# Optimization experiments

Hardware: AMD Instinct MI355X
Metric: run time of the kernel (lower is better)

Reference implementation:

```python
import jax, jax.numpy as jnp
import numpy as np
from jax import lax

DIM = 64
HEADS = 8
B, H, W = 4, 256, 256


def layer_norm(x, w, b):
    # WithBias LayerNorm over channel dim (dim=1 of NCHW), per-pixel
    mu = jnp.mean(x, axis=1, keepdims=True)
    var = jnp.mean((x - mu) ** 2, axis=1, keepdims=True)
    xn = (x - mu) / jnp.sqrt(var + 1e-5)
    return xn * w[None, :, None, None] + b[None, :, None, None]


def conv1x1(x, w, b=None):
    out = jnp.einsum('oc,bchw->bohw', w, x)
    if b is not None:
        out = out + b[None, :, None, None]
    return out


def dwconv3x3(x, w):
    # w: [C,1,3,3], depthwise (groups=C), stride 1, pad 1
    return lax.conv_general_dilated(
        x, w, window_strides=(1, 1), padding=((1, 1), (1, 1)),
        feature_group_count=x.shape[1],
        dimension_numbers=('NCHW', 'OIHW', 'NCHW'))


def modulation(v, y, mw, mb):
    # mw: [4, C, C] = [scale0, scale1, shift0, shift1]; mb: [4, C]
    s = conv1x1(jax.nn.leaky_relu(conv1x1(y, mw[0], mb[0]), 0.1), mw[1], mb[1])
    t = conv1x1(jax.nn.leaky_relu(conv1x1(y, mw[2], mb[2]), 0.1), mw[3], mb[3])
    return v * (s + 1.0) + t


def _heads(t):
    b, c, h, w = t.shape
    return t.reshape(b, HEADS, c // HEADS, h * w)


def channel_attn(q, k, v, temp):
    b, c, h, w = v.shape
    q, k, v = _heads(q), _heads(k), _heads(v)  # b, head, ch, hw
    q = q / jnp.maximum(jnp.linalg.norm(q, axis=-1, keepdims=True), 1e-12)
    k = k / jnp.maximum(jnp.linalg.norm(k, axis=-1, keepdims=True), 1e-12)
    attn = jnp.einsum('bhcn,bhdn->bhcd', q, k) * temp[None]  # small CxC
    attn = jax.nn.softmax(attn, axis=-1)
    out = jnp.einsum('bhcd,bhdn->bhcn', attn, v)
    return out.reshape(b, c, h, w)


def setup_inputs() -> dict:
    key = jax.random.key(0)
    ks = jax.random.split(key, 24)
    sc = 0.05
    d = {
        'x': jax.random.normal(ks[0], (B, DIM, H, W), jnp.float32),
        'y': jax.random.normal(ks[1], (B, DIM, H, W), jnp.float32),
        'ln_w': jnp.ones((DIM,), jnp.float32),
        'ln_b': jnp.zeros((DIM,), jnp.float32),
        'temp': jnp.ones((HEADS, 1, 1), jnp.float32),
        'kv1_w': jax.random.normal(ks[2], (2 * DIM, DIM), jnp.float32) * sc,
        'kvdw1_w': jax.random.normal(ks[3], (2 * DIM, 1, 3, 3), jnp.float32) * sc,
        'q1_w': jax.random.normal(ks[4], (DIM, DIM), jnp.float32) * sc,
        'qdw1_w': jax.random.normal(ks[5], (DIM, 1, 3, 3), jnp.float32) * sc,
        'po1_w': jax.random.normal(ks[6], (DIM, DIM), jnp.float32) * sc,
        'kv2_w': jax.random.normal(ks[7], (2 * DIM, DIM), jnp.float32) * sc,
        'kvdw2_w': jax.random.normal(ks[8], (2 * DIM, 1, 3, 3), jnp.float32) * sc,
        'q2_w': jax.random.normal(ks[9], (DIM, DIM), jnp.float32) * sc,
        'qdw2_w': jax.random.normal(ks[10], (DIM, 1, 3, 3), jnp.float32) * sc,
        'po2_w': jax.random.normal(ks[11], (DIM, DIM), jnp.float32) * sc,
        'mm1_w': jax.random.normal(ks[12], (4, DIM, DIM), jnp.float32) * sc,
        'mm1_b': jnp.zeros((4, DIM), jnp.float32),
        'mm2_w': jax.random.normal(ks[13], (4, DIM, DIM), jnp.float32) * sc,
        'mm2_b': jnp.zeros((4, DIM), jnp.float32),
    }
    return d


def reference(x, y, ln_w, ln_b, temp,
              kv1_w, kvdw1_w, q1_w, qdw1_w, po1_w,
              kv2_w, kvdw2_w, q2_w, qdw2_w, po2_w,
              mm1_w, mm1_b, mm2_w, mm2_b):
    x1 = layer_norm(x, ln_w, ln_b)
    y1 = layer_norm(y, ln_w, ln_b)  # original reuses self.norm1 for both

    # branch 1: kv from x1, q from y1, v modulated by x, residual y
    kv1 = dwconv3x3(conv1x1(x1, kv1_w), kvdw1_w)
    k1, v1 = jnp.split(kv1, 2, axis=1)
    q1 = dwconv3x3(conv1x1(y1, q1_w), qdw1_w)
    v1 = modulation(v1, x, mm1_w, mm1_b)
    out1 = conv1x1(channel_attn(q1, k1, v1, temp), po1_w) + y

    # branch 2: kv from y1, q from x1, v modulated by y, residual x
    kv2 = dwconv3x3(conv1x1(y1, kv2_w), kvdw2_w)
    k2, v2 = jnp.split(kv2, 2, axis=1)
    q2 = dwconv3x3(conv1x1(x1, q2_w), qdw2_w)
    v2 = modulation(v2, y, mm2_w, mm2_b)
    out2 = conv1x1(channel_attn(q2, k2, v2, temp), po2_w) + x

    return (out1, out2)
```

## Files before the change

kernel.cpp:

```cpp
#include <hip/hip_runtime.h>
#include <hip/hip_bf16.h>

#define HW 65536
#define BATCH 4
#define NPIX (BATCH*HW)

typedef unsigned short u16;
typedef unsigned int   u32;
typedef __attribute__((ext_vector_type(8))) short bh8;
typedef __attribute__((ext_vector_type(4))) float f4;

__device__ __forceinline__ float b2f(u16 u){
    u32 i = ((u32)u) << 16; float f; __builtin_memcpy(&f, &i, 4); return f;
}
__device__ __forceinline__ u16 f2b(float f){
    __hip_bfloat16 h = __float2bfloat16(f); u16 u; __builtin_memcpy(&u, &h, 2); return u;
}

__device__ __forceinline__ f4 mfma16(bh8 a, bh8 b, f4 c){
    return __builtin_amdgcn_mfma_f32_16x16x32_bf16(a, b, c, 0, 0, 0);
}

struct CvtJob { const float* src; u16* dst; int n; const float* cs; };
struct SetupArgs {
    CvtJob j[12];
    const float* kvw[2]; const float* qw[2];
    const float* lnw; const float* lnb;
    float* sums; float* lnc;
};
__global__ __launch_bounds__(256) void setup_kernel(SetupArgs S){
    int blk = blockIdx.x;
    if (blk < 12){
        const CvtJob J = S.j[blk];
        if (J.cs){
            for (int i = threadIdx.x; i < J.n; i += 256) J.dst[i] = f2b(J.src[i] * J.cs[i & 63]);
        } else {
            for (int i = threadIdx.x; i < J.n; i += 256) J.dst[i] = f2b(J.src[i]);
        }
        return;
    }
    int pb = blk - 12;
    if (pb == 0){
        for (int i = threadIdx.x; i < 5120; i += 256) S.sums[i] = 0.f;
    } else if (pb <= 2){
        const float* W = S.kvw[pb-1];
        float* rs = S.lnc + (pb-1)*256;
        int o = threadIdx.x;
        if (o < 128){
            float a = 0.f, bb = 0.f;
            for (int c = 0; c < 64; c++){
                float wv = W[o*64 + c];
                a = fmaf(wv, S.lnw[c], a); bb = fmaf(wv, S.lnb[c], bb);
            }
            rs[o] = a; rs[128 + o] = bb;
        }
    } else {
        const float* W = S.qw[pb-3];
        float* rs = S.lnc + 512 + (pb-3)*128;
        int o = threadIdx.x;
        if (o < 64){
            float a = 0.f, bb = 0.f;
            for (int c = 0; c < 64; c++){
                float wv = W[o*64 + c];
                a = fmaf(wv, S.lnw[c], a); bb = fmaf(wv, S.lnb[c], bb);
            }
            rs[o] = a; rs[64 + o] = bb;
        }
    }
}

struct GemmDual {
    const float* in[2];
    const u16* wa[2];
    const float* rs[2]; const float* rb[2];
    u16* outLo[2]; u16* outHi[2];
};
template<int MT>
__global__ __launch_bounds__(256) void gemmln_kernel(GemmDual G){
    constexpr int KD = 64;
    constexpr int NW = MT*16*KD;
    __shared__ u16 wl[NW];
    int seg = blockIdx.x >> 10, tile = blockIdx.x & 1023;
    int w = threadIdx.x >> 6, lane = threadIdx.x & 63;
    int quad = lane >> 4, l16 = lane & 15;
    int b = tile >> 8;
    int pbase = ((tile & 255) << 8) + (w << 6) + (l16 << 2);

    const float* in = G.in[seg];
    f4 fin[8];
    #pragma unroll
    for (int j = 0; j < 8; j++)
        fin[j] = *(const f4*)(in + ((size_t)b*64 + quad*8 + j)*HW + pbase);

    {
        const u16* W = G.wa[seg];
        for (int i = threadIdx.x; i < NW/8; i += 256){
            int row = i >> 3, ch = i & 7;
            uint4 v = *(const uint4*)(W + row*KD + ch*8);
            *(uint4*)(wl + row*KD + ((ch ^ (row & 7)) << 3)) = v;
        }
    }
    __syncthreads();

    f4 fin2[8];
    #pragma unroll
    for (int j = 0; j < 8; j++)
        fin2[j] = *(const f4*)(in + ((size_t)b*64 + 32 + quad*8 + j)*HW + pbase);

    float s1[4] = {0.f,0.f,0.f,0.f}, s2[4] = {0.f,0.f,0.f,0.f};
    f4 acc[MT][4];
    #pragma unroll
    for (int mi = 0; mi < MT; mi++)
        #pragma unroll
        for (int p = 0; p < 4; p++) acc[mi][p] = (f4){0.f,0.f,0.f,0.f};

    #pragma unroll
    for (int ks = 0; ks < 2; ks++){
        bh8 bfr[4];
        #pragma unroll
        for (int j = 0; j < 8; j++){
            f4 fv = (ks == 0) ? fin[j] : fin2[j];
            #pragma unroll
            for (int p = 0; p < 4; p++){
                float v = fv[p];
                s1[p] += v; s2[p] = fmaf(v, v, s2[p]);
                bfr[p][j] = (short)f2b(v);
            }
        }
        #pragma unroll
        for (int mi = 0; mi < MT; mi++){
            bh8 a;
            __builtin_memcpy(&a, wl + (mi*16 + l16)*KD + ((((ks<<2)+quad) ^ (l16 & 7)) << 3), 16);
            #pragma unroll
            for (int p = 0; p < 4; p++)
                acc[mi][p] = mfma16(a, bfr[p], acc[mi][p]);
        }
    }

    float mu[4], iv[4];
    #pragma unroll
    for (int p = 0; p < 4; p++){
        s1[p] += __shfl_xor(s1[p], 16); s1[p] += __shfl_xor(s1[p], 32);
        s2[p] += __shfl_xor(s2[p], 16); s2[p] += __shfl_xor(s2[p], 32);
        mu[p] = s1[p]*(1.f/64.f);
        iv[p] = rsqrtf(s2[p]*(1.f/64.f) - mu[p]*mu[p] + 1e-5f);
    }

    const float* rs = G.rs[seg]; const float* rb = G.rb[seg];
    u16* oLo = G.outLo[seg]; u16* oHi = G.outHi[seg];
    #pragma unroll
    for (int mi = 0; mi < MT; mi++)
    #pragma unroll
    for (int r = 0; r < 4; r++){
        int o = mi*16 + quad*4 + r;
        size_t pidx = ((size_t)b*64 + (o & 63))*HW + pbase;
        float rsv = rs[o], rbv = rb[o];
        float v0 = iv[0]*(acc[mi][0][r] - mu[0]*rsv) + rbv;
        float v1 = iv[1]*(acc[mi][1][r] - mu[1]*rsv) + rbv;
        float v2 = iv[2]*(acc[mi][2][r] - mu[2]*rsv) + rbv;
        float v3 = iv[3]*(acc[mi][3][r] - mu[3]*rsv) + rbv;
        uint2 st;
        st.x = (u32)f2b(v0) | ((u32)f2b(v1) << 16);
        st.y = (u32)f2b(v2) | ((u32)f2b(v3) << 16);
        u16* dst = (o < 64) ? oLo : oHi;
        *(uint2*)(dst + pidx) = st;
    }
}

struct Dw6 { const u16* in[6]; u16* out[6]; const float* w[6]; int choff[6]; };
__global__ __launch_bounds__(256) void dw6_kernel(Dw6 A){
    int seg = blockIdx.x >> 13;
    int lid = ((blockIdx.x & 8191) << 8) + threadIdx.x;
    const u16* inp = A.in[seg];
    u16* outp      = A.out[seg];
    const float* wd = A.w[seg];
    int choff      = A.choff[seg];
    int bc = lid >> 13;
    int n8 = lid & 8191;
    int h = n8 >> 5, c8 = (n8 & 31) << 3;
    const float* wc = wd + ((size_t)((bc & 63) + choff))*9;
    const u16* p = inp + (size_t)bc*HW;
    float row[3][10];
    #pragma unroll
    for (int r = 0; r < 3; r++){
        int hh = h - 1 + r;
        bool ok = (unsigned)hh < 256u;
        const u16* pr = p + hh*256 + c8;
        if (ok){
            uint4 m = *(const uint4*)pr;
            row[r][1] = b2f((u16)m.x); row[r][2] = b2f((u16)(m.x>>16));
            row[r][3] = b2f((u16)m.y); row[r][4] = b2f((u16)(m.y>>16));
            row[r][5] = b2f((u16)m.z); row[r][6] = b2f((u16)(m.z>>16));
            row[r][7] = b2f((u16)m.w); row[r][8] = b2f((u16)(m.w>>16));
            row[r][0] = (c8 > 0)   ? b2f(pr[-1]) : 0.f;
            row[r][9] = (c8 < 248) ? b2f(pr[8])  : 0.f;
        } else {
            #pragma unroll
            for (int j = 0; j < 10; j++) row[r][j] = 0.f;
        }
    }
    float o[8];
    #pragma unroll
    for (int i = 0; i < 8; i++){
        float a = 0.f;
        #pragma unroll
        for (int r = 0; r < 3; r++){
            a = fmaf(wc[r*3+0], row[r][i],   a);
            a = fmaf(wc[r*3+1], row[r][i+1], a);
            a = fmaf(wc[r*3+2], row[r][i+2], a);
        }
        o[i] = a;
    }
    uint4 st;
    st.x = (u32)f2b(o[0]) | ((u32)f2b(o[1])<<16);
    st.y = (u32)f2b(o[2]) | ((u32)f2b(o[3])<<16);
    st.z = (u32)f2b(o[4]) | ((u32)f2b(o[5])<<16);
    st.w = (u32)f2b(o[6]) | ((u32)f2b(o[7])<<16);
    *(uint4*)(outp + (size_t)bc*HW + h*256 + c8) = st;
}

#define NSL 64
struct AttnDual { const u16* q[2]; const u16* k[2]; float* sums; };
__global__ __launch_bounds__(256) void attn_part_kernel(AttnDual AD){
    int seg = blockIdx.x >> 11;
    int blk = blockIdx.x & 2047;
    int sl = blk & (NSL-1);
    int bh = blk >> 6;
    int b = bh >> 3, h = bh & 7;
    const u16* qp = AD.q[seg] + ((size_t)b*64 + h*8)*HW + sl*(HW/NSL);
    const u16* kp = AD.k[seg] + ((size_t)b*64 + h*8)*HW + sl*(HW/NSL);
    float acc[80];
    #pragma unroll
    for (int i = 0; i < 80; i++) acc[i] = 0.f;
    int n0 = threadIdx.x << 2;
    float qv[8][4], kw[8][4];
    #pragma unroll
    for (int i = 0; i < 8; i++){
        uint2 mq = *(const uint2*)(qp + (size_t)i*HW + n0);
        uint2 mk = *(const uint2*)(kp + (size_t)i*HW + n0);
        qv[i][0] = b2f((u16)(mq.x & 0xffffu)); qv[i][1] = b2f((u16)(mq.x >> 16));
        qv[i][2] = b2f((u16)(mq.y & 0xffffu)); qv[i][3] = b2f((u16)(mq.y >> 16));
        kw[i][0] = b2f((u16)(mk.x & 0xffffu)); kw[i][1] = b2f((u16)(mk.x >> 16));
        kw[i][2] = b2f((u16)(mk.y & 0xffffu)); kw[i][3] = b2f((u16)(mk.y >> 16));
    }
    #pragma unroll
    for (int i = 0; i < 8; i++){
        #pragma unroll
        for (int u = 0; u < 4; u++){
            acc[64+i] = fmaf(qv[i][u], qv[i][u], acc[64+i]);
            acc[72+i] = fmaf(kw[i][u], kw[i][u], acc[72+i]);
        }
        #pragma unroll
        for (int j = 0; j < 8; j++)
            #pragma unroll
            for (int u = 0; u < 4; u++)
                acc[i*8+j] = fmaf(qv[i][u], kw[j][u], acc[i*8+j]);
    }
    __shared__ float sred[4][80];
    int lane = threadIdx.x & 63, wv = threadIdx.x >> 6;
    #pragma unroll
    for (int t = 0; t < 80; t++){
        float r = acc[t];
        r += __shfl_down(r, 32); r += __shfl_down(r, 16); r += __shfl_down(r, 8);
        r += __shfl_down(r, 4);  r += __shfl_down(r, 2);  r += __shfl_down(r, 1);
        if (lane == 0) sred[wv][t] = r;
    }
    __syncthreads();
    if (threadIdx.x < 80){
        int t = threadIdx.x;
        atomicAdd(&AD.sums[seg*2560 + bh*80 + t], sred[0][t]+sred[1][t]+sred[2][t]+sred[3][t]);
    }
}

struct WeffDual { const float* sums; const float* temp; const float* po[2]; u16* weff[2]; };
__global__ __launch_bounds__(64) void weff_kernel(WeffDual WD){
    int seg = blockIdx.x >> 2;
    int b = blockIdx.x & 3;
    const float* po = WD.po[seg];
    u16* weff = WD.weff[seg];
    __shared__ float at[8][8][8];
    int t = threadIdx.x;
    {
        int h = t >> 3, i = t & 7;
        const float* f = WD.sums + seg*2560 + (b*8 + h)*80;
        float iq = 1.f / fmaxf(sqrtf(f[64+i]), 1e-12f);
        float tv = WD.temp[h];
        float row[8]; float m = -1e30f;
        #pragma unroll
        for (int j = 0; j < 8; j++){
            float ik = 1.f / fmaxf(sqrtf(f[72+j]), 1e-12f);
            row[j] = f[i*8+j]*iq*ik*tv;
            m = fmaxf(m, row[j]);
        }
        float s = 0.f;
        #pragma unroll
        for (int j = 0; j < 8; j++){ row[j] = expf(row[j]-m); s += row[j]; }
        float rsv = 1.f/s;
        #pragma unroll
        for (int j = 0; j < 8; j++) at[h][i][j] = row[j]*rsv;
    }
    __syncthreads();
    int o = t;
    for (int g = 0; g < 64; g++){
        int h = g >> 3, j = g & 7;
        float wv = 0.f;
        #pragma unroll
        for (int i = 0; i < 8; i++) wv = fmaf(po[o*64 + h*8 + i], at[h][i][j], wv);
        weff[b*4096 + o*64 + g] = f2b(wv);
    }
}

struct ModFinal {
    const float* in[2]; const u16* wa[2]; const u16* wb[2];
    const float* b0[2]; const float* b2[2]; const float* b1[2]; const float* b3[2];
    const u16* wf[2];
    const u16* v[2];
    const float* resid[2];
    float* out[2];
};
__global__ __launch_bounds__(256) void modfinal_kernel(ModFinal M){
    __shared__ u32 lds[128*128];
    int seg = blockIdx.x >> 10, tile = blockIdx.x & 1023;
    int w = threadIdx.x >> 6, lane = threadIdx.x & 63;
    int quad = lane >> 4, l16 = lane & 15;
    int b = tile >> 8;
    int pbase = ((tile & 255) << 8) + (w << 6) + (l16 << 2);
    int pp = ((w << 4) + l16) << 1;

    const float* in = M.in[seg];
    const u16* wa = M.wa[seg];

    f4 fin[8], fin2[8];
    #pragma unroll
    for (int j = 0; j < 8; j++)
        fin[j] = *(const f4*)(in + ((size_t)b*64 + quad*8 + j)*HW + pbase);
    #pragma unroll
    for (int j = 0; j < 8; j++)
        fin2[j] = *(const f4*)(in + ((size_t)b*64 + 32 + quad*8 + j)*HW + pbase);

    f4 acc[8][4];
    #pragma unroll
    for (int mi = 0; mi < 8; mi++)
        #pragma unroll
        for (int p = 0; p < 4; p++) acc[mi][p] = (f4){0.f,0.f,0.f,0.f};

    #pragma unroll
    for (int ks = 0; ks < 2; ks++){
        bh8 bfr[4];
        #pragma unroll
        for (int j = 0; j < 8; j++){
            f4 fv = (ks == 0) ? fin[j] : fin2[j];
            #pragma unroll
            for (int p = 0; p < 4; p++) bfr[p][j] = (short)f2b(fv[p]);
        }
        #pragma unroll
        for (int mi = 0; mi < 8; mi++){
            bh8 a;
            __builtin_memcpy(&a, wa + (mi*16 + l16)*64 + ks*32 + quad*8, 16);
            #pragma unroll
            for (int p = 0; p < 4; p++)
                acc[mi][p] = mfma16(a, bfr[p], acc[mi][p]);
        }
    }

    uint2 vpref[16];
    {
        const u16* vP = M.v[seg];
        #pragma unroll
        for (int mi = 0; mi < 4; mi++)
        #pragma unroll
        for (int r = 0; r < 4; r++)
            vpref[mi*4+r] = *(const uint2*)(vP + ((size_t)b*64 + mi*16 + quad*4 + r)*HW + pbase);
    }

    {
        const float* b0v = M.b0[seg]; const float* b2v = M.b2[seg];
        #pragma unroll
        for (int mi = 0; mi < 8; mi++)
        #pragma unroll
        for (int r = 0; r < 4; r++){
            int o = mi*16 + quad*4 + r;
            float bi = (o < 64) ? b0v[o] : b2v[o-64];
            float v0 = acc[mi][0][r] + bi; v0 = v0 > 0.f ? v0 : 0.1f*v0;
            float v1 = acc[mi][1][r] + bi; v1 = v1 > 0.f ? v1 : 0.1f*v1;
            float v2 = acc[mi][2][r] + bi; v2 = v2 > 0.f ? v2 : 0.1f*v2;
            float v3 = acc[mi][3][r] + bi; v3 = v3 > 0.f ? v3 : 0.1f*v3;
            uint2 st;
            st.x = (u32)f2b(v0) | ((u32)f2b(v1) << 16);
            st.y = (u32)f2b(v2) | ((u32)f2b(v3) << 16);
            *(uint2*)&lds[o*128 + ((pp + ((o>>2)&3)*8) & 127)] = st;
        }
    }
    __syncthreads();

    const u16* wb = M.wb[seg];
    f4 acc2[8][4];
    #pragma unroll
    for (int mi = 0; mi < 8; mi++)
        #pragma unroll
        for (int p = 0; p < 4; p++) acc2[mi][p] = (f4){0.f,0.f,0.f,0.f};
    #pragma unroll
    for (int ks = 0; ks < 4; ks++){
        int kb = ks*32 + quad*8;
        bh8 bfr[4];
        #pragma unroll
        for (int j = 0; j < 8; j++){
            int ch = kb + j;
            uint2 m = *(const uint2*)&lds[ch*128 + ((pp + ((ch>>2)&3)*8) & 127)];
            bfr[0][j] = (short)(m.x & 0xffffu);
            bfr[1][j] = (short)(m.x >> 16);
            bfr[2][j] = (short)(m.y & 0xffffu);
            bfr[3][j] = (short)(m.y >> 16);
        }
        #pragma unroll
        for (int mi = 0; mi < 8; mi++){
            if (mi < 4 ? (ks < 2) : (ks >= 2)){
                int ksl = (mi >= 4) ? ks - 2 : ks;
                bh8 a;
                __builtin_memcpy(&a, wb + (mi*16 + l16)*64 + ksl*32 + quad*8, 16);
                #pragma unroll
                for (int p = 0; p < 4; p++)
                    acc2[mi][p] = mfma16(a, bfr[p], acc2[mi][p]);
            }
        }
    }
    __syncthreads();

    {
        const float* b1v = M.b1[seg]; const float* b3v = M.b3[seg];
        #pragma unroll
        for (int mi = 0; mi < 4; mi++)
        #pragma unroll
        for (int r = 0; r < 4; r++){
            int o = mi*16 + quad*4 + r;
            uint2 vv = vpref[mi*4+r];
            float va[4] = { b2f((u16)(vv.x & 0xffffu)), b2f((u16)(vv.x >> 16)),
                            b2f((u16)(vv.y & 0xffffu)), b2f((u16)(vv.y >> 16)) };
            float ov[4];
            #pragma unroll
            for (int p = 0; p < 4; p++){
                float s = acc2[mi][p][r] + b1v[o];
                float t = acc2[mi+4][p][r] + b3v[o];
                ov[p] = va[p]*(s+1.f)+t;
            }
            uint2 st;
            st.x = (u32)f2b(ov[0]) | ((u32)f2b(ov[1]) << 16);
            st.y = (u32)f2b(ov[2]) | ((u32)f2b(ov[3]) << 16);
            *(uint2*)&lds[o*128 + ((pp + ((o>>2)&3)*8) & 127)] = st;
        }
    }
    f4 rpre[16];
    {
        const float* resid = M.resid[seg];
        #pragma unroll
        for (int mi = 0; mi < 4; mi++)
        #pragma unroll
        for (int r = 0; r < 4; r++)
            rpre[mi*4+r] = *(const f4*)(resid + ((size_t)b*64 + mi*16 + quad*4 + r)*HW + pbase);
    }
    __syncthreads();

    const u16* wf = M.wf[seg] + b*4096;
    f4 accF[4][4];
    #pragma unroll
    for (int mi = 0; mi < 4; mi++)
        #pragma unroll
        for (int p = 0; p < 4; p++) accF[mi][p] = (f4){0.f,0.f,0.f,0.f};
    #pragma unroll
    for (int ks = 0; ks < 2; ks++){
        int kb = ks*32 + quad*8;
        bh8 bfr[4];
        #pragma unroll
        for (int j = 0; j < 8; j++){
            int ch = kb + j;
            uint2 m = *(const uint2*)&lds[ch*128 + ((pp + ((ch>>2)&3)*8) & 127)];
            bfr[0][j] = (short)(m.x & 0xffffu);
            bfr[1][j] = (short)(m.x >> 16);
            bfr[2][j] = (short)(m.y & 0xffffu);
            bfr[3][j] = (short)(m.y >> 16);
        }
        #pragma unroll
        for (int mi = 0; mi < 4; mi++){
            bh8 a;
            __builtin_memcpy(&a, wf + (mi*16 + l16)*64 + ks*32 + quad*8, 16);
            #pragma unroll
            for (int p = 0; p < 4; p++)
                accF[mi][p] = mfma16(a, bfr[p], accF[mi][p]);
        }
    }
    {
        float* outF = M.out[seg];
        #pragma unroll
        for (int mi = 0; mi < 4; mi++)
        #pragma unroll
        for (int r = 0; r < 4; r++){
            int o = mi*16 + quad*4 + r;
            size_t pidx = ((size_t)b*64 + o)*HW + pbase;
            f4 rr = rpre[mi*4+r];
            f4 st;
            #pragma unroll
            for (int p = 0; p < 4; p++) st[p] = accF[mi][p][r] + rr[p];
            *(f4*)(outF + pidx) = st;
        }
    }
}

extern "C" void kernel_launch(void* const* d_in, const int* in_sizes, int n_in,
                              void* d_out, int out_size, void* d_ws, size_t ws_size,
                              hipStream_t stream){
    const float* x    = (const float*)d_in[0];
    const float* y    = (const float*)d_in[1];
    const float* ln_w = (const float*)d_in[2];
    const float* ln_b = (const float*)d_in[3];
    const float* temp = (const float*)d_in[4];
    const float* kv_w[2]   = {(const float*)d_in[5],  (const float*)d_in[10]};
    const float* kvdw_w[2] = {(const float*)d_in[6],  (const float*)d_in[11]};
    const float* q_w[2]    = {(const float*)d_in[7],  (const float*)d_in[12]};
    const float* qdw_w[2]  = {(const float*)d_in[8],  (const float*)d_in[13]};
    const float* po_w[2]   = {(const float*)d_in[9],  (const float*)d_in[14]};
    const float* mm_w[2]   = {(const float*)d_in[15], (const float*)d_in[17]};
    const float* mm_b[2]   = {(const float*)d_in[16], (const float*)d_in[18]};

    const size_t HPE = (size_t)BATCH*64*HW;
    u16* PL = (u16*)d_ws;
    u16* P[12];
    for (int i = 0; i < 12; i++) P[i] = PL + (size_t)i*HPE;
    float* sums = (float*)(PL + 12*HPE);
    float* lnc  = sums + 5120;
    u16* warena = (u16*)(lnc + 768);
    const int WKV[2] = {0, 8192}, WQ[2] = {16384, 20480};
    const int WMA[2] = {24576, 40960}, WMB[2] = {32768, 49152};
    const int WEFF[2] = {57344, 73728};

    size_t need = 12*HPE*2 + (5120+768)*4 + 90112*2;
    if (ws_size < need) return;

    SetupArgs S{};
    int nj = 0;
    auto add = [&](const float* s, u16* d, int n, const float* cs){ S.j[nj] = {s, d, n, cs}; nj++; };
    for (int br = 0; br < 2; br++){
        add(kv_w[br],        warena + WKV[br],        8192, ln_w);
        add(q_w[br],         warena + WQ[br],         4096, ln_w);
        add(mm_w[br],        warena + WMA[br],        4096, nullptr);
        add(mm_w[br]+8192,   warena + WMA[br] + 4096, 4096, nullptr);
        add(mm_w[br]+4096,   warena + WMB[br],        4096, nullptr);
        add(mm_w[br]+12288,  warena + WMB[br] + 4096, 4096, nullptr);
    }
    S.kvw[0] = kv_w[0]; S.kvw[1] = kv_w[1];
    S.qw[0]  = q_w[0];  S.qw[1]  = q_w[1];
    S.lnw = ln_w; S.lnb = ln_b; S.sums = sums; S.lnc = lnc;
    setup_kernel<<<17, 256, 0, stream>>>(S);

    const int GT = NPIX/256;

    GemmDual GK{};
    GK.in[0] = x; GK.in[1] = y;
    GK.wa[0] = warena + WKV[0]; GK.wa[1] = warena + WKV[1];
    GK.rs[0] = lnc;        GK.rb[0] = lnc + 128;
    GK.rs[1] = lnc + 256;  GK.rb[1] = lnc + 384;
    GK.outLo[0] = P[0]; GK.outHi[0] = P[1];
    GK.outLo[1] = P[2]; GK.outHi[1] = P[3];
    gemmln_kernel<8><<<2*GT, 256, 0, stream>>>(GK);

    GemmDual GQ{};
    GQ.in[0] = y; GQ.in[1] = x;
    GQ.wa[0] = warena + WQ[0]; GQ.wa[1] = warena + WQ[1];
    GQ.rs[0] = lnc + 512;  GQ.rb[0] = lnc + 576;
    GQ.rs[1] = lnc + 640;  GQ.rb[1] = lnc + 704;
    GQ.outLo[0] = P[4]; GQ.outHi[0] = P[4];
    GQ.outLo[1] = P[5]; GQ.outHi[1] = P[5];
    gemmln_kernel<4><<<2*GT, 256, 0, stream>>>(GQ);

    Dw6 D{};
    D.in[0] = P[0];  D.out[0] = P[6];  D.w[0] = kvdw_w[0]; D.choff[0] = 0;
    D.in[1] = P[1];  D.out[1] = P[7];  D.w[1] = kvdw_w[0]; D.choff[1] = 64;
    D.in[2] = P[4];  D.out[2] = P[8];  D.w[2] = qdw_w[0];  D.choff[2] = 0;
    D.in[3] = P[2];  D.out[3] = P[9];  D.w[3] = kvdw_w[1]; D.choff[3] = 0;
    D.in[4] = P[3];  D.out[4] = P[10]; D.w[4] = kvdw_w[1]; D.choff[4] = 64;
    D.in[5] = P[5];  D.out[5] = P[11]; D.w[5] = qdw_w[1];  D.choff[5] = 0;
    dw6_kernel<<<6*8192, 256, 0, stream>>>(D);

    AttnDual AD{};
    AD.q[0] = P[8];  AD.k[0] = P[6];
    AD.q[1] = P[11]; AD.k[1] = P[9];
    AD.sums = sums;
    attn_part_kernel<<<2*BATCH*8*NSL, 256, 0, stream>>>(AD);

    WeffDual WD{};
    WD.sums = sums; WD.temp = temp;
    WD.po[0] = po_w[0]; WD.po[1] = po_w[1];
    WD.weff[0] = warena + WEFF[0]; WD.weff[1] = warena + WEFF[1];
    weff_kernel<<<2*BATCH, 64, 0, stream>>>(WD);

    float* outp = (float*)d_out;
    ModFinal M{};
    M.in[0] = x; M.in[1] = y;
    M.wa[0] = warena + WMA[0]; M.wa[1] = warena + WMA[1];
    M.wb[0] = warena + WMB[0]; M.wb[1] = warena + WMB[1];
    M.b0[0] = mm_b[0];       M.b0[1] = mm_b[1];
    M.b2[0] = mm_b[0] + 128; M.b2[1] = mm_b[1] + 128;
    M.b1[0] = mm_b[0] + 64;  M.b1[1] = mm_b[1] + 64;
    M.b3[0] = mm_b[0] + 192; M.b3[1] = mm_b[1] + 192;
    M.wf[0] = warena + WEFF[0]; M.wf[1] = warena + WEFF[1];
    M.v[0] = P[7]; M.v[1] = P[10];
    M.resid[0] = y; M.resid[1] = x;
    M.out[0] = outp; M.out[1] = outp + HPE;
    modfinal_kernel<<<2*GT, 256, 0, stream>>>(M);
}
```

Baseline: 694.8 us.

## Merge KV and Q layernorm-GEMMs into one kernel per input; use shuffles for dwconv halos

The separate KV (128 outputs) and Q (64 outputs) LayerNorm+1x1-conv kernels are fused into one kernel that computes all 192 output channels from a single read of each fp32 input, so x and y are each loaded and normalized once instead of twice. Weights and LN correction sums are regrouped per input (kv of one branch plus q of the other), and the MFMA loop is restructured to finish and store one 16-row tile at a time to bound accumulator registers. The depthwise conv also replaces its scalar halo loads with lane shuffles. The merged kernel uses more shared memory (24KB) and a longer per-block loop, which may lower occupancy.

```diff
diff --git a/kernel.cpp b/kernel.cpp
--- a/kernel.cpp
+++ b/kernel.cpp
@@ -42,44 +42,30 @@
     int pb = blk - 12;
     if (pb == 0){
         for (int i = threadIdx.x; i < 5120; i += 256) S.sums[i] = 0.f;
-    } else if (pb <= 2){
-        const float* W = S.kvw[pb-1];
-        float* rs = S.lnc + (pb-1)*256;
+    } else {
+        int seg = pb - 1;
         int o = threadIdx.x;
-        if (o < 128){
+        if (o < 192){
+            const float* W = (o < 128) ? S.kvw[seg] : S.qw[1-seg];
+            int row = (o < 128) ? o : o - 128;
             float a = 0.f, bb = 0.f;
             for (int c = 0; c < 64; c++){
-                float wv = W[o*64 + c];
+                float wv = W[row*64 + c];
                 a = fmaf(wv, S.lnw[c], a); bb = fmaf(wv, S.lnb[c], bb);
             }
-            rs[o] = a; rs[128 + o] = bb;
-        }
-    } else {
-        const float* W = S.qw[pb-3];
-        float* rs = S.lnc + 512 + (pb-3)*128;
-        int o = threadIdx.x;
-        if (o < 64){
-            float a = 0.f, bb = 0.f;
-            for (int c = 0; c < 64; c++){
-                float wv = W[o*64 + c];
-                a = fmaf(wv, S.lnw[c], a); bb = fmaf(wv, S.lnb[c], bb);
-            }
-            rs[o] = a; rs[64 + o] = bb;
-        }
-    }
-}
-
-struct GemmDual {
+            S.lnc[seg*384 + o] = a; S.lnc[seg*384 + 192 + o] = bb;
+        }
+    }
+}
+
+struct GemmMerged {
     const float* in[2];
     const u16* wa[2];
     const float* rs[2]; const float* rb[2];
-    u16* outLo[2]; u16* outHi[2];
+    u16* out0[2]; u16* out1[2]; u16* out2[2];
 };
-template<int MT>
-__global__ __launch_bounds__(256) void gemmln_kernel(GemmDual G){
-    constexpr int KD = 64;
-    constexpr int NW = MT*16*KD;
-    __shared__ u16 wl[NW];
+__global__ __launch_bounds__(256) void gemmln_kernel(GemmMerged G){
+    __shared__ u16 wl[192*64];
     int seg = blockIdx.x >> 10, tile = blockIdx.x & 1023;
     int w = threadIdx.x >> 6, lane = threadIdx.x & 63;
     int quad = lane >> 4, l16 = lane & 15;
@@ -87,53 +73,44 @@
     int pbase = ((tile & 255) << 8) + (w << 6) + (l16 << 2);
 
     const float* in = G.in[seg];
-    f4 fin[8];
+    f4 fin[8], fin2[8];
     #pragma unroll
     for (int j = 0; j < 8; j++)
         fin[j] = *(const f4*)(in + ((size_t)b*64 + quad*8 + j)*HW + pbase);
-
-    {
-        const u16* W = G.wa[seg];
-        for (int i = threadIdx.x; i < NW/8; i += 256){
-            int row = i >> 3, ch = i & 7;
-            uint4 v = *(const uint4*)(W + row*KD + ch*8);
-            *(uint4*)(wl + row*KD + ((ch ^ (row & 7)) << 3)) = v;
-        }
-    }
-    __syncthreads();
-
-    f4 fin2[8];
     #pragma unroll
     for (int j = 0; j < 8; j++)
         fin2[j] = *(const f4*)(in + ((size_t)b*64 + 32 + quad*8 + j)*HW + pbase);
 
+    {
+        const u16* W = G.wa[seg];
+        for (int i = threadIdx.x; i < 192*8; i += 256){
+            int row = i >> 3, ch = i & 7;
+            uint4 v = *(const uint4*)(W + row*64 + ch*8);
+            *(uint4*)(wl + row*64 + ((ch ^ (row & 7)) << 3)) = v;
+        }
+    }
+    __syncthreads();
+
     float s1[4] = {0.f,0.f,0.f,0.f}, s2[4] = {0.f,0.f,0.f,0.f};
-    f4 acc[MT][4];
-    #pragma unroll
-    for (int mi = 0; mi < MT; mi++)
-        #pragma unroll
-        for (int p = 0; p < 4; p++) acc[mi][p] = (f4){0.f,0.f,0.f,0.f};
-
-    #pragma unroll
-    for (int ks = 0; ks < 2; ks++){
-        bh8 bfr[4];
-        #pragma unroll
-        for (int j = 0; j < 8; j++){
-            f4 fv = (ks == 0) ? fin[j] : fin2[j];
-            #pragma unroll
-            for (int p = 0; p < 4; p++){
-                float v = fv[p];
-                s1[p] += v; s2[p] = fmaf(v, v, s2[p]);
-                bfr[p][j] = (short)f2b(v);
-            }
-        }
-        #pragma unroll
-        for (int mi = 0; mi < MT; mi++){
-            bh8 a;
-            __builtin_memcpy(&a, wl + (mi*16 + l16)*KD + ((((ks<<2)+quad) ^ (l16 & 7)) << 3), 16);
-            #pragma unroll
-            for (int p = 0; p < 4; p++)
-                acc[mi][p] = mfma16(a, bfr[p], acc[mi][p]);
+    bh8 bfr[2][4];
+    #pragma unroll
+    for (int j = 0; j < 8; j++){
+        f4 fv = fin[j];
+        #pragma unroll
+        for (int p = 0; p < 4; p++){
+            float v = fv[p];
+            s1[p] += v; s2[p] = fmaf(v, v, s2[p]);
+            bfr[0][p][j] = (short)f2b(v);
+        }
+    }
+    #pragma unroll
+    for (int j = 0; j < 8; j++){
+        f4 fv = fin2[j];
+        #pragma unroll
+        for (int p = 0; p < 4; p++){
+            float v = fv[p];
+            s1[p] += v; s2[p] = fmaf(v, v, s2[p]);
+            bfr[1][p][j] = (short)f2b(v);
         }
     }
 
@@ -147,23 +124,35 @@
     }
 
     const float* rs = G.rs[seg]; const float* rb = G.rb[seg];
-    u16* oLo = G.outLo[seg]; u16* oHi = G.outHi[seg];
-    #pragma unroll
-    for (int mi = 0; mi < MT; mi++)
-    #pragma unroll
-    for (int r = 0; r < 4; r++){
-        int o = mi*16 + quad*4 + r;
-        size_t pidx = ((size_t)b*64 + (o & 63))*HW + pbase;
-        float rsv = rs[o], rbv = rb[o];
-        float v0 = iv[0]*(acc[mi][0][r] - mu[0]*rsv) + rbv;
-        float v1 = iv[1]*(acc[mi][1][r] - mu[1]*rsv) + rbv;
-        float v2 = iv[2]*(acc[mi][2][r] - mu[2]*rsv) + rbv;
-        float v3 = iv[3]*(acc[mi][3][r] - mu[3]*rsv) + rbv;
-        uint2 st;
-        st.x = (u32)f2b(v0) | ((u32)f2b(v1) << 16);
-        st.y = (u32)f2b(v2) | ((u32)f2b(v3) << 16);
-        u16* dst = (o < 64) ? oLo : oHi;
-        *(uint2*)(dst + pidx) = st;
+    u16* o0 = G.out0[seg]; u16* o1 = G.out1[seg]; u16* o2 = G.out2[seg];
+    #pragma unroll
+    for (int mi = 0; mi < 12; mi++){
+        f4 acc[4];
+        #pragma unroll
+        for (int p = 0; p < 4; p++) acc[p] = (f4){0.f,0.f,0.f,0.f};
+        #pragma unroll
+        for (int ks = 0; ks < 2; ks++){
+            bh8 a;
+            __builtin_memcpy(&a, wl + (mi*16 + l16)*64 + ((((ks<<2)+quad) ^ (l16 & 7)) << 3), 16);
+            #pragma unroll
+            for (int p = 0; p < 4; p++)
+                acc[p] = mfma16(a, bfr[ks][p], acc[p]);
+        }
+        u16* dst = (mi < 4) ? o0 : (mi < 8) ? o1 : o2;
+        #pragma unroll
+        for (int r = 0; r < 4; r++){
+            int o = mi*16 + quad*4 + r;
+            size_t pidx = ((size_t)b*64 + (o & 63))*HW + pbase;
+            float rsv = rs[o], rbv = rb[o];
+            float v0 = iv[0]*(acc[0][r] - mu[0]*rsv) + rbv;
+            float v1 = iv[1]*(acc[1][r] - mu[1]*rsv) + rbv;
+            float v2 = iv[2]*(acc[2][r] - mu[2]*rsv) + rbv;
+            float v3 = iv[3]*(acc[3][r] - mu[3]*rsv) + rbv;
+            uint2 st;
+            st.x = (u32)f2b(v0) | ((u32)f2b(v1) << 16);
+            st.y = (u32)f2b(v2) | ((u32)f2b(v3) << 16);
+            *(uint2*)(dst + pidx) = st;
+        }
     }
 }
 
@@ -192,12 +181,14 @@
             row[r][3] = b2f((u16)m.y); row[r][4] = b2f((u16)(m.y>>16));
             row[r][5] = b2f((u16)m.z); row[r][6] = b2f((u16)(m.z>>16));
             row[r][7] = b2f((u16)m.w); row[r][8] = b2f((u16)(m.w>>16));
-            row[r][0] = (c8 > 0)   ? b2f(pr[-1]) : 0.f;
-            row[r][9] = (c8 < 248) ? b2f(pr[8])  : 0.f;
         } else {
             #pragma unroll
-            for (int j = 0; j < 10; j++) row[r][j] = 0.f;
-        }
+            for (int j = 1; j < 9; j++) row[r][j] = 0.f;
+        }
+        float lft = __shfl_up(row[r][8], 1);
+        float rgt = __shfl_down(row[r][1], 1);
+        row[r][0] = (c8 > 0)   ? lft : 0.f;
+        row[r][9] = (c8 < 248) ? rgt : 0.f;
     }
     float o[8];
     #pragma unroll
@@ -528,7 +519,7 @@
     float* sums = (float*)(PL + 12*HPE);
     float* lnc  = sums + 5120;
     u16* warena = (u16*)(lnc + 768);
-    const int WKV[2] = {0, 8192}, WQ[2] = {16384, 20480};
+    const int WG[2] = {0, 12288};
     const int WMA[2] = {24576, 40960}, WMB[2] = {32768, 49152};
     const int WEFF[2] = {57344, 73728};
 
@@ -538,9 +529,11 @@
     SetupArgs S{};
     int nj = 0;
     auto add = [&](const float* s, u16* d, int n, const float* cs){ S.j[nj] = {s, d, n, cs}; nj++; };
+    add(kv_w[0], warena + WG[0],        8192, ln_w);
+    add(q_w[1],  warena + WG[0] + 8192, 4096, ln_w);
+    add(kv_w[1], warena + WG[1],        8192, ln_w);
+    add(q_w[0],  warena + WG[1] + 8192, 4096, ln_w);
     for (int br = 0; br < 2; br++){
-        add(kv_w[br],        warena + WKV[br],        8192, ln_w);
-        add(q_w[br],         warena + WQ[br],         4096, ln_w);
         add(mm_w[br],        warena + WMA[br],        4096, nullptr);
         add(mm_w[br]+8192,   warena + WMA[br] + 4096, 4096, nullptr);
         add(mm_w[br]+4096,   warena + WMB[br],        4096, nullptr);
@@ -549,27 +542,18 @@
     S.kvw[0] = kv_w[0]; S.kvw[1] = kv_w[1];
     S.qw[0]  = q_w[0];  S.qw[1]  = q_w[1];
     S.lnw = ln_w; S.lnb = ln_b; S.sums = sums; S.lnc = lnc;
-    setup_kernel<<<17, 256, 0, stream>>>(S);
+    setup_kernel<<<15, 256, 0, stream>>>(S);
 
     const int GT = NPIX/256;
 
-    GemmDual GK{};
+    GemmMerged GK{};
     GK.in[0] = x; GK.in[1] = y;
-    GK.wa[0] = warena + WKV[0]; GK.wa[1] = warena + WKV[1];
-    GK.rs[0] = lnc;        GK.rb[0] = lnc + 128;
-    GK.rs[1] = lnc + 256;  GK.rb[1] = lnc + 384;
-    GK.outLo[0] = P[0]; GK.outHi[0] = P[1];
-    GK.outLo[1] = P[2]; GK.outHi[1] = P[3];
-    gemmln_kernel<8><<<2*GT, 256, 0, stream>>>(GK);
-
-    GemmDual GQ{};
-    GQ.in[0] = y; GQ.in[1] = x;
-    GQ.wa[0] = warena + WQ[0]; GQ.wa[1] = warena + WQ[1];
-    GQ.rs[0] = lnc + 512;  GQ.rb[0] = lnc + 576;
-    GQ.rs[1] = lnc + 640;  GQ.rb[1] = lnc + 704;
-    GQ.outLo[0] = P[4]; GQ.outHi[0] = P[4];
-    GQ.outLo[1] = P[5]; GQ.outHi[1] = P[5];
-    gemmln_kernel<4><<<2*GT, 256, 0, stream>>>(GQ);
+    GK.wa[0] = warena + WG[0]; GK.wa[1] = warena + WG[1];
+    GK.rs[0] = lnc;        GK.rb[0] = lnc + 192;
+    GK.rs[1] = lnc + 384;  GK.rb[1] = lnc + 576;
+    GK.out0[0] = P[0]; GK.out1[0] = P[1]; GK.out2[0] = P[5];
+    GK.out0[1] = P[2]; GK.out1[1] = P[3]; GK.out2[1] = P[4];
+    gemmln_kernel<<<2*GT, 256, 0, stream>>>(GK);
 
     Dw6 D{};
     D.in[0] = P[0];  D.out[0] = P[6];  D.w[0] = kvdw_w[0]; D.choff[0] = 0;
```

Measured after the change: 611.7 us. 12.0% less time.
